# Kernel optimization log

Measured on AMD Instinct MI355X. Metric: run time of the kernel, lower is better.

## Reference

```python
import jax, jax.numpy as jnp
import numpy as np

B, RES, DIM, H, KD = 16, 32, 768, 12, 64
N = RES * RES          # 1024 tokens
D = KD                 # attn_ratio = 1 -> per-head value dim == key_dim
DH = D * H             # 768
SCALE = KD ** -0.5
LN_EPS = 1e-5


def _bias_idxs():
    # replicate the itertools.product construction: for row-major points,
    # offsets (|dy|,|dx|) are first seen in order dy-major, so id = |dy|*RES + |dx|
    coords = np.arange(N)
    y, x = coords // RES, coords % RES
    dy = np.abs(y[:, None] - y[None, :])
    dx = np.abs(x[:, None] - x[None, :])
    return jnp.asarray(dy * RES + dx, dtype=jnp.int32)  # [N, N]


def setup_inputs() -> dict:
    key = jax.random.key(0)
    ks = jax.random.split(key, 8)
    return {
        "x": jax.random.normal(ks[0], (B, N, DIM), jnp.float32),
        "ln_w": 1.0 + 0.01 * jax.random.normal(ks[1], (DIM,), jnp.float32),
        "ln_b": 0.01 * jax.random.normal(ks[2], (DIM,), jnp.float32),
        "qkv_w": 0.02 * jax.random.normal(ks[3], (3 * H * KD, DIM), jnp.float32),
        "qkv_b": 0.01 * jax.random.normal(ks[4], (3 * H * KD,), jnp.float32),
        "proj_w": 0.02 * jax.random.normal(ks[5], (DIM, DH), jnp.float32),
        "proj_b": 0.01 * jax.random.normal(ks[6], (DIM,), jnp.float32),
        "attn_biases": 0.1 * jax.random.normal(ks[7], (H, RES * RES), jnp.float32),
        "bias_idxs": _bias_idxs(),
    }


def reference(x, ln_w, ln_b, qkv_w, qkv_b, proj_w, proj_b, attn_biases, bias_idxs):
    # LayerNorm over the feature dim
    mu = jnp.mean(x, axis=-1, keepdims=True)
    var = jnp.mean(jnp.square(x - mu), axis=-1, keepdims=True)
    xn = (x - mu) * jax.lax.rsqrt(var + LN_EPS) * ln_w + ln_b

    # fused qkv projection -> [B, N, H, 3*KD], split per head
    qkv = (xn @ qkv_w.T + qkv_b).reshape(B, N, H, 3 * KD)
    q, k, v = jnp.split(qkv, [KD, 2 * KD], axis=3)  # each [B, N, H, KD]

    # gathered relative-position bias: [H, N, N]
    bias = attn_biases[:, bias_idxs]

    # scores + bias -> softmax -> AV
    attn = jnp.einsum("bnhk,bmhk->bhnm", q, k) * SCALE + bias[None]
    attn = jax.nn.softmax(attn, axis=-1)
    out = jnp.einsum("bhnm,bmhd->bnhd", attn, v).reshape(B, N, DH)
    return out @ proj_w.T + proj_b
```

## Files before the change

### kernel.cpp

```cpp
#include <hip/hip_runtime.h>
#include <cstdint>
#include <cstddef>

#define AS1 __attribute__((address_space(1)))
#define AS3 __attribute__((address_space(3)))

typedef float f32x4 __attribute__((ext_vector_type(4)));
typedef __bf16 bf16x8 __attribute__((ext_vector_type(8)));
typedef __bf16 bf16x4 __attribute__((ext_vector_type(4)));
typedef uint32_t u32x4 __attribute__((ext_vector_type(4)));

__device__ __forceinline__ void async_cp16(void* lds, const void* g) {
    __builtin_amdgcn_global_load_lds((AS1 void*)(g), (AS3 void*)(lds), 16, 0, 0);
}

__device__ __forceinline__ bf16x8 frag_of(u32x4 u) {
    return __builtin_bit_cast(bf16x8, u);
}

__global__ __launch_bounds__(256)
void cvt_w(const float* __restrict__ qkvw, const float* __restrict__ projw,
           __bf16* __restrict__ qkvwb, __bf16* __restrict__ projwb) {
    int i = blockIdx.x * 256 + threadIdx.x;
    if (i < 442368) {
        int row = i / 192, c4 = (i - row * 192) * 4;
        int t = (row >= 1536) ? 2 : (row >= 768 ? 1 : 0);
        int rem = row - t * 768;
        int hh = rem >> 6, d = rem & 63;
        int in_row = hh * 192 + t * 64 + d;
        float4 v = *(const float4*)(qkvw + (long)in_row * 768 + c4);
        bf16x4 o;
        o[0] = (__bf16)v.x; o[1] = (__bf16)v.y; o[2] = (__bf16)v.z; o[3] = (__bf16)v.w;
        *(bf16x4*)(qkvwb + (long)row * 768 + c4) = o;
    } else {
        int j = i - 442368;
        float4 v = ((const float4*)projw)[j];
        bf16x4 o;
        o[0] = (__bf16)v.x; o[1] = (__bf16)v.y; o[2] = (__bf16)v.z; o[3] = (__bf16)v.w;
        ((bf16x4*)projwb)[j] = o;
    }
}

__global__ __launch_bounds__(256)
void ln_kernel(const float* __restrict__ x, const float* __restrict__ w,
               const float* __restrict__ bsh, __bf16* __restrict__ xn) {
    const int lane = threadIdx.x & 63;
    const long row = (long)blockIdx.x * 4 + (threadIdx.x >> 6);
    const float4* xr = (const float4*)(x + row * 768);
    float4 v[3];
    v[0] = xr[lane]; v[1] = xr[lane + 64]; v[2] = xr[lane + 128];
    float s = 0.f, ss = 0.f;
#pragma unroll
    for (int i = 0; i < 3; ++i) {
        s  += v[i].x + v[i].y + v[i].z + v[i].w;
        ss += v[i].x * v[i].x + v[i].y * v[i].y + v[i].z * v[i].z + v[i].w * v[i].w;
    }
#pragma unroll
    for (int m = 1; m < 64; m <<= 1) { s += __shfl_xor(s, m); ss += __shfl_xor(ss, m); }
    const float mean = s * (1.f / 768.f);
    const float rstd = rsqrtf(ss * (1.f / 768.f) - mean * mean + 1e-5f);
    const float4* wv = (const float4*)w;
    const float4* bv = (const float4*)bsh;
    bf16x4* outp = (bf16x4*)(xn + row * 768);
#pragma unroll
    for (int i = 0; i < 3; ++i) {
        float4 wi = wv[lane + 64 * i], bi = bv[lane + 64 * i];
        bf16x4 o;
        o[0] = (__bf16)((v[i].x - mean) * rstd * wi.x + bi.x);
        o[1] = (__bf16)((v[i].y - mean) * rstd * wi.y + bi.y);
        o[2] = (__bf16)((v[i].z - mean) * rstd * wi.z + bi.z);
        o[3] = (__bf16)((v[i].w - mean) * rstd * wi.w + bi.w);
        outp[lane + 64 * i] = o;
    }
}

template <int MODE>
__device__ __forceinline__
void gemm_core(__bf16* As, __bf16* Bs,
               const __bf16* __restrict__ A, const __bf16* __restrict__ Bw,
               const float* __restrict__ bias,
               __bf16* __restrict__ q_out, __bf16* __restrict__ k_out,
               __bf16* __restrict__ vt_out, float* __restrict__ f_out,
               long bm, long bn) {
    constexpr int K = 768;
    const int tid  = threadIdx.x;
    const int lane = tid & 63;
    const int quad = lane >> 4;
    const int l16  = lane & 15;
    const int wave = tid >> 6;
    const int wm = wave >> 1, wn = wave & 1;

    const __bf16* Ab = A  + bm * K;
    const __bf16* Bb = Bw + bn * K;

    const int el0 = tid, el1 = tid + 256;
    const int rA0 = el0 >> 2, rA1 = el1 >> 2;
    const int kc  = (tid & 3) * 8;

    f32x4 acc[4][4] = {};

    for (int k0 = 0; k0 < K; k0 += 32) {
        __syncthreads();
        async_cp16((char*)As + el0 * 16, Ab + (long)rA0 * K + (k0 + kc));
        async_cp16((char*)As + el1 * 16, Ab + (long)rA1 * K + (k0 + kc));
        async_cp16((char*)Bs + el0 * 16, Bb + (long)rA0 * K + (k0 + kc));
        async_cp16((char*)Bs + el1 * 16, Bb + (long)rA1 * K + (k0 + kc));
        __syncthreads();

        const u32x4* Av = (const u32x4*)As;
        const u32x4* Bv = (const u32x4*)Bs;
        bf16x8 af[4], bfr[4];
#pragma unroll
        for (int t = 0; t < 4; ++t) {
            af[t]  = frag_of(Av[(wm * 64 + t * 16 + l16) * 4 + quad]);
            bfr[t] = frag_of(Bv[(wn * 64 + t * 16 + l16) * 4 + quad]);
        }
#pragma unroll
        for (int i = 0; i < 4; ++i)
#pragma unroll
            for (int j = 0; j < 4; ++j) {
                if constexpr (MODE == 0)
                    acc[i][j] = __builtin_amdgcn_mfma_f32_16x16x32_bf16(bfr[j], af[i], acc[i][j], 0, 0, 0);
                else
                    acc[i][j] = __builtin_amdgcn_mfma_f32_16x16x32_bf16(af[i], bfr[j], acc[i][j], 0, 0, 0);
            }
    }

    if constexpr (MODE == 0) {
#pragma unroll
        for (int j = 0; j < 4; ++j) {
            int col0 = (int)bn + wn * 64 + j * 16 + quad * 4;
            int t  = col0 >= 768;
            int cc = col0 - t * 768;
            int h  = cc >> 6, d = cc & 63;
            int f  = h * 192 + t * 64 + d;
            float4 bb = *(const float4*)(bias + f);
            __bf16* dst = t ? k_out : q_out;
#pragma unroll
            for (int i = 0; i < 4; ++i) {
                long row = bm + wm * 64 + i * 16 + l16;
                long b   = row >> 10;
                long n   = row & 1023;
                bf16x4 pk;
                pk[0] = (__bf16)(acc[i][j][0] + bb.x);
                pk[1] = (__bf16)(acc[i][j][1] + bb.y);
                pk[2] = (__bf16)(acc[i][j][2] + bb.z);
                pk[3] = (__bf16)(acc[i][j][3] + bb.w);
                *(bf16x4*)(dst + ((b * 12 + h) * 1024 + n) * 64 + d) = pk;
            }
        }
    } else if constexpr (MODE == 2) {
#pragma unroll
        for (int j = 0; j < 4; ++j) {
            int cv = (int)bn - 1536 + wn * 64 + j * 16 + l16;
            int h  = cv >> 6, d = cv & 63;
            float bv = bias[h * 192 + 128 + d];
#pragma unroll
            for (int i = 0; i < 4; ++i) {
                long row0 = bm + wm * 64 + i * 16 + quad * 4;
                long b    = row0 >> 10;
                long n0   = row0 & 1023;
                bf16x4 pk;
                pk[0] = (__bf16)(acc[i][j][0] + bv);
                pk[1] = (__bf16)(acc[i][j][1] + bv);
                pk[2] = (__bf16)(acc[i][j][2] + bv);
                pk[3] = (__bf16)(acc[i][j][3] + bv);
                *(bf16x4*)(vt_out + ((b * 12 + h) * 64 + d) * 1024 + n0) = pk;
            }
        }
    } else {
#pragma unroll
        for (int i = 0; i < 4; ++i) {
#pragma unroll
            for (int r = 0; r < 4; ++r) {
                long row = bm + wm * 64 + i * 16 + quad * 4 + r;
#pragma unroll
                for (int j = 0; j < 4; ++j) {
                    int col = (int)bn + wn * 64 + j * 16 + l16;
                    f_out[row * 768 + col] = acc[i][j][r] + bias[col];
                }
            }
        }
    }
}

__global__ __launch_bounds__(256, 2)
void gemm_qkv(const __bf16* __restrict__ A, const __bf16* __restrict__ Bw,
              const float* __restrict__ bias, __bf16* __restrict__ qb,
              __bf16* __restrict__ kb, __bf16* __restrict__ vtb) {
    __shared__ __align__(16) __bf16 As[128 * 32];
    __shared__ __align__(16) __bf16 Bs[128 * 32];
    int blk = blockIdx.x;
    int bx = blk % 18;
    long by = blk / 18;
    if (bx < 12)
        gemm_core<0>(As, Bs, A, Bw, bias, qb, kb, nullptr, nullptr, by * 128, (long)bx * 128);
    else
        gemm_core<2>(As, Bs, A, Bw, bias, nullptr, nullptr, vtb, nullptr, by * 128, (long)bx * 128);
}

__global__ __launch_bounds__(256, 2)
void gemm_proj(const __bf16* __restrict__ A, const __bf16* __restrict__ Bw,
               const float* __restrict__ bias, float* __restrict__ out) {
    __shared__ __align__(16) __bf16 As[128 * 32];
    __shared__ __align__(16) __bf16 Bs[128 * 32];
    gemm_core<1>(As, Bs, A, Bw, bias, nullptr, nullptr, nullptr, out,
                 (long)blockIdx.y * 128, (long)blockIdx.x * 128);
}

__global__ __launch_bounds__(256, 4)
void attn_kernel(const __bf16* __restrict__ Q, const __bf16* __restrict__ Kb,
                 const __bf16* __restrict__ Vt, const float* __restrict__ biases,
                 __bf16* __restrict__ out) {
    __shared__ __align__(16) __bf16 QPs[128 * 64];
    __shared__ __align__(16) __bf16 Ks[64 * 64];
    __shared__ __align__(16) __bf16 Vts[64 * 64];
    __shared__ __align__(16) float brow[1024];

    const int tid  = threadIdx.x;
    const int lane = tid & 63;
    const int wave = tid >> 6;
    const int quad = lane >> 4;
    const int l16  = lane & 15;
    const int sw   = l16 & 7;
    const int qt = blockIdx.x;
    const int h  = blockIdx.y;
    const int b  = blockIdx.z;

    const long bh = (long)b * 12 + h;
    const __bf16* Qg  = Q  + (bh * 1024 + qt * 128) * 64;
    const __bf16* Kg  = Kb + bh * 1024 * 64;
    const __bf16* Vtg = Vt + bh * 64 * 1024;

#pragma unroll
    for (int p = 0; p < 4; ++p) {
        int e = tid + p * 256, r = e >> 3, c = (e & 7) ^ (r & 7);
        async_cp16((char*)QPs + e * 16, Qg + r * 64 + c * 8);
    }
    {
        const float LOG2E = 1.4426950408889634f;
        float4 v = ((const float4*)(biases + (long)h * 1024))[tid];
        float4 o; o.x = v.x * LOG2E; o.y = v.y * LOG2E; o.z = v.z * LOG2E; o.w = v.w * LOG2E;
        ((float4*)brow)[tid] = o;
    }
    __syncthreads();

    bf16x8 aq[2][2];
    {
        const u32x4* Qv = (const u32x4*)QPs;
#pragma unroll
        for (int g = 0; g < 2; ++g) {
            int qrow = wave * 32 + g * 16 + l16;
            aq[g][0] = frag_of(Qv[qrow * 8 + (quad ^ sw)]);
            aq[g][1] = frag_of(Qv[qrow * 8 + ((quad + 4) ^ sw)]);
        }
    }

    const int yq = qt * 4 + wave;
    int pdxb[2][2][4];
#pragma unroll
    for (int g = 0; g < 2; ++g)
#pragma unroll
        for (int i2 = 0; i2 < 2; ++i2)
#pragma unroll
            for (int r = 0; r < 4; ++r) {
                int d = (g * 16 + l16) - (i2 * 16 + quad * 4 + r);
                pdxb[g][i2][r] = (d < 0 ? -d : d) * 4;
            }

    const float SSCALE = 0.125f * 1.4426950408889634f;
    float lacc[2] = {0.f, 0.f};
    f32x4 o[2][4] = {};
    __bf16* Psw = QPs + wave * 2048;

    const int e0 = tid, e1 = tid + 256;
    const int r0 = e0 >> 3, c0 = (e0 & 7) ^ (r0 & 7);
    const int r1 = e1 >> 3, c1 = (e1 & 7) ^ (r1 & 7);

    for (int kt = 0; kt < 16; ++kt) {
        __syncthreads();
        {
            const __bf16* Kt  = Kg + kt * 4096;
            const __bf16* Vtt = Vtg + kt * 64;
            async_cp16((char*)Ks + e0 * 16, Kt + r0 * 64 + c0 * 8);
            async_cp16((char*)Ks + e1 * 16, Kt + r1 * 64 + c1 * 8);
            async_cp16((char*)Vts + e0 * 16, Vtt + r0 * 1024 + c0 * 8);
            async_cp16((char*)Vts + e1 * 16, Vtt + r1 * 1024 + c1 * 8);
        }
        __syncthreads();

        f32x4 s[2][4];
        const u32x4* Kv = (const u32x4*)Ks;
#pragma unroll
        for (int nt = 0; nt < 4; ++nt) {
            int krow = nt * 16 + l16;
            bf16x8 k0 = frag_of(Kv[krow * 8 + (quad ^ sw)]);
            bf16x8 k1 = frag_of(Kv[krow * 8 + ((quad + 4) ^ sw)]);
#pragma unroll
            for (int g = 0; g < 2; ++g) {
                f32x4 z = {0.f, 0.f, 0.f, 0.f};
                z = __builtin_amdgcn_mfma_f32_16x16x32_bf16(k0, aq[g][0], z, 0, 0, 0);
                z = __builtin_amdgcn_mfma_f32_16x16x32_bf16(k1, aq[g][1], z, 0, 0, 0);
                s[g][nt] = z;
            }
        }

        int dy0 = yq - 2 * kt;     dy0 = dy0 < 0 ? -dy0 : dy0;
        int dy1 = yq - 2 * kt - 1; dy1 = dy1 < 0 ? -dy1 : dy1;
        const char* br0 = (const char*)(brow + dy0 * 32);
        const char* br1 = (const char*)(brow + dy1 * 32);
#pragma unroll
        for (int g = 0; g < 2; ++g) {
            int rowb = (g * 16 + l16) * 128 + (quad & 1) * 8;
#pragma unroll
            for (int nt = 0; nt < 4; ++nt) {
                const char* br = (nt & 2) ? br1 : br0;
                bf16x4 pk;
#pragma unroll
                for (int r = 0; r < 4; ++r) {
                    float bvv = *(const float*)(br + pdxb[g][nt & 1][r]);
                    float p = __builtin_amdgcn_exp2f(s[g][nt][r] * SSCALE + bvv);
                    lacc[g] += p;
                    pk[r] = (__bf16)p;
                }
                *(bf16x4*)((char*)Psw + rowb + (((nt * 2 + (quad >> 1)) ^ sw) << 4)) = pk;
            }
        }

        const u32x4* Pv = (const u32x4*)Psw;
        const u32x4* Vv = (const u32x4*)Vts;
        bf16x8 bp[2][2];
#pragma unroll
        for (int g = 0; g < 2; ++g) {
            int prow = g * 16 + l16;
            bp[g][0] = frag_of(Pv[prow * 8 + (quad ^ sw)]);
            bp[g][1] = frag_of(Pv[prow * 8 + ((quad + 4) ^ sw)]);
        }
#pragma unroll
        for (int dt = 0; dt < 4; ++dt) {
            int vrow = dt * 16 + l16;
            bf16x8 v0 = frag_of(Vv[vrow * 8 + (quad ^ sw)]);
            bf16x8 v1 = frag_of(Vv[vrow * 8 + ((quad + 4) ^ sw)]);
#pragma unroll
            for (int g = 0; g < 2; ++g) {
                o[g][dt] = __builtin_amdgcn_mfma_f32_16x16x32_bf16(v0, bp[g][0], o[g][dt], 0, 0, 0);
                o[g][dt] = __builtin_amdgcn_mfma_f32_16x16x32_bf16(v1, bp[g][1], o[g][dt], 0, 0, 0);
            }
        }
    }

#pragma unroll
    for (int g = 0; g < 2; ++g) {
        float l = lacc[g];
        l += __shfl_xor(l, 16);
        l += __shfl_xor(l, 32);
        const float rl = 1.f / l;
        const long n = qt * 128 + wave * 32 + g * 16 + l16;
        __bf16* op = out + ((long)b * 1024 + n) * 768 + h * 64 + quad * 4;
#pragma unroll
        for (int dt = 0; dt < 4; ++dt) {
            bf16x4 ov;
            ov[0] = (__bf16)(o[g][dt][0] * rl);
            ov[1] = (__bf16)(o[g][dt][1] * rl);
            ov[2] = (__bf16)(o[g][dt][2] * rl);
            ov[3] = (__bf16)(o[g][dt][3] * rl);
            *(bf16x4*)(op + dt * 16) = ov;
        }
    }
}

extern "C" void kernel_launch(void* const* d_in, const int* in_sizes, int n_in,
                              void* d_out, int out_size, void* d_ws, size_t ws_size,
                              hipStream_t stream) {
    (void)in_sizes; (void)n_in; (void)out_size; (void)ws_size;
    const float* x      = (const float*)d_in[0];
    const float* ln_w   = (const float*)d_in[1];
    const float* ln_b   = (const float*)d_in[2];
    const float* qkv_w  = (const float*)d_in[3];
    const float* qkv_b  = (const float*)d_in[4];
    const float* proj_w = (const float*)d_in[5];
    const float* proj_b = (const float*)d_in[6];
    const float* ab     = (const float*)d_in[7];
    float* outp = (float*)d_out;

    char* ws = (char*)d_ws;
    __bf16* xn     = (__bf16*)(ws);
    __bf16* aout   = (__bf16*)(ws);
    __bf16* qkvwb  = (__bf16*)(ws + 25165824);
    __bf16* projwb = (__bf16*)(ws + 28704768);
    __bf16* qb     = (__bf16*)(ws + 29884416);
    __bf16* kb     = (__bf16*)(ws + 55050240);
    __bf16* vtb    = (__bf16*)(ws + 80216064);

    cvt_w<<<2304, 256, 0, stream>>>(qkv_w, proj_w, qkvwb, projwb);
    ln_kernel<<<4096, 256, 0, stream>>>(x, ln_w, ln_b, xn);
    gemm_qkv<<<2304, 256, 0, stream>>>(xn, qkvwb, qkv_b, qb, kb, vtb);
    attn_kernel<<<dim3(8, 12, 16), 256, 0, stream>>>(qb, kb, vtb, ab, aout);
    gemm_proj<<<dim3(6, 128), 256, 0, stream>>>(aout, projwb, proj_b, outp);
}
```

Measured before the change: 348.3 us.

## Halve attention query tile to 64 rows, store bias in fp16, raise occupancy bounds

The attention kernel now handles 64 query rows per block instead of 128, with each wave owning 16 rows, and the grid doubles to compensate. The per-head bias row moves from fp32 to fp16 in LDS, and the Q/P buffer is halved, cutting LDS and register use so launch bounds can rise to 6 blocks per CU. The GEMM launch bounds also go from 2 to 3 blocks. In exchange, each K/V tile loaded into LDS is reused by half as many queries, which doubles K/V traffic, and the fp16 bias adds a small rounding error.

After: 333.7 us. -4.2%, faster.

```diff
diff --git a/kernel.cpp b/kernel.cpp
--- a/kernel.cpp
+++ b/kernel.cpp
@@ -8,6 +8,7 @@
 typedef float f32x4 __attribute__((ext_vector_type(4)));
 typedef __bf16 bf16x8 __attribute__((ext_vector_type(8)));
 typedef __bf16 bf16x4 __attribute__((ext_vector_type(4)));
+typedef _Float16 h16x4 __attribute__((ext_vector_type(4)));
 typedef uint32_t u32x4 __attribute__((ext_vector_type(4)));
 
 __device__ __forceinline__ void async_cp16(void* lds, const void* g) {
@@ -184,7 +185,7 @@
     }
 }
 
-__global__ __launch_bounds__(256, 2)
+__global__ __launch_bounds__(256, 3)
 void gemm_qkv(const __bf16* __restrict__ A, const __bf16* __restrict__ Bw,
               const float* __restrict__ bias, __bf16* __restrict__ qb,
               __bf16* __restrict__ kb, __bf16* __restrict__ vtb) {
@@ -199,7 +200,7 @@
         gemm_core<2>(As, Bs, A, Bw, bias, nullptr, nullptr, vtb, nullptr, by * 128, (long)bx * 128);
 }
 
-__global__ __launch_bounds__(256, 2)
+__global__ __launch_bounds__(256, 3)
 void gemm_proj(const __bf16* __restrict__ A, const __bf16* __restrict__ Bw,
                const float* __restrict__ bias, float* __restrict__ out) {
     __shared__ __align__(16) __bf16 As[128 * 32];
@@ -208,14 +209,14 @@
                  (long)blockIdx.y * 128, (long)blockIdx.x * 128);
 }
 
-__global__ __launch_bounds__(256, 4)
+__global__ __launch_bounds__(256, 6)
 void attn_kernel(const __bf16* __restrict__ Q, const __bf16* __restrict__ Kb,
                  const __bf16* __restrict__ Vt, const float* __restrict__ biases,
                  __bf16* __restrict__ out) {
-    __shared__ __align__(16) __bf16 QPs[128 * 64];
+    __shared__ __align__(16) __bf16 QPs[64 * 64];
     __shared__ __align__(16) __bf16 Ks[64 * 64];
     __shared__ __align__(16) __bf16 Vts[64 * 64];
-    __shared__ __align__(16) float brow[1024];
+    __shared__ __align__(16) _Float16 brow[1024];
 
     const int tid  = threadIdx.x;
     const int lane = tid & 63;
@@ -228,54 +229,50 @@
     const int b  = blockIdx.z;
 
     const long bh = (long)b * 12 + h;
-    const __bf16* Qg  = Q  + (bh * 1024 + qt * 128) * 64;
+    const __bf16* Qg  = Q  + (bh * 1024 + qt * 64) * 64;
     const __bf16* Kg  = Kb + bh * 1024 * 64;
     const __bf16* Vtg = Vt + bh * 64 * 1024;
 
-#pragma unroll
-    for (int p = 0; p < 4; ++p) {
-        int e = tid + p * 256, r = e >> 3, c = (e & 7) ^ (r & 7);
-        async_cp16((char*)QPs + e * 16, Qg + r * 64 + c * 8);
-    }
+    const int e0 = tid, e1 = tid + 256;
+    const int r0 = e0 >> 3, c0 = (e0 & 7) ^ (r0 & 7);
+    const int r1 = e1 >> 3, c1 = (e1 & 7) ^ (r1 & 7);
+
+    async_cp16((char*)QPs + e0 * 16, Qg + r0 * 64 + c0 * 8);
+    async_cp16((char*)QPs + e1 * 16, Qg + r1 * 64 + c1 * 8);
     {
         const float LOG2E = 1.4426950408889634f;
         float4 v = ((const float4*)(biases + (long)h * 1024))[tid];
-        float4 o; o.x = v.x * LOG2E; o.y = v.y * LOG2E; o.z = v.z * LOG2E; o.w = v.w * LOG2E;
-        ((float4*)brow)[tid] = o;
+        h16x4 o;
+        o[0] = (_Float16)(v.x * LOG2E); o[1] = (_Float16)(v.y * LOG2E);
+        o[2] = (_Float16)(v.z * LOG2E); o[3] = (_Float16)(v.w * LOG2E);
+        *(h16x4*)(brow + tid * 4) = o;
     }
     __syncthreads();
 
-    bf16x8 aq[2][2];
+    bf16x8 aq[2];
     {
         const u32x4* Qv = (const u32x4*)QPs;
-#pragma unroll
-        for (int g = 0; g < 2; ++g) {
-            int qrow = wave * 32 + g * 16 + l16;
-            aq[g][0] = frag_of(Qv[qrow * 8 + (quad ^ sw)]);
-            aq[g][1] = frag_of(Qv[qrow * 8 + ((quad + 4) ^ sw)]);
-        }
-    }
-
-    const int yq = qt * 4 + wave;
-    int pdxb[2][2][4];
-#pragma unroll
-    for (int g = 0; g < 2; ++g)
-#pragma unroll
-        for (int i2 = 0; i2 < 2; ++i2)
-#pragma unroll
-            for (int r = 0; r < 4; ++r) {
-                int d = (g * 16 + l16) - (i2 * 16 + quad * 4 + r);
-                pdxb[g][i2][r] = (d < 0 ? -d : d) * 4;
-            }
+        int qrow = wave * 16 + l16;
+        aq[0] = frag_of(Qv[qrow * 8 + (quad ^ sw)]);
+        aq[1] = frag_of(Qv[qrow * 8 + ((quad + 4) ^ sw)]);
+    }
+
+    const int yq = 2 * qt + (wave >> 1);
+    const int xq = ((wave & 1) << 4) + l16;
+    int pdx[2][4];
+#pragma unroll
+    for (int i2 = 0; i2 < 2; ++i2)
+#pragma unroll
+        for (int r = 0; r < 4; ++r) {
+            int xk = (i2 << 4) + quad * 4 + r;
+            int d = xq - xk; pdx[i2][r] = d < 0 ? -d : d;
+        }
 
     const float SSCALE = 0.125f * 1.4426950408889634f;
-    float lacc[2] = {0.f, 0.f};
-    f32x4 o[2][4] = {};
-    __bf16* Psw = QPs + wave * 2048;
-
-    const int e0 = tid, e1 = tid + 256;
-    const int r0 = e0 >> 3, c0 = (e0 & 7) ^ (r0 & 7);
-    const int r1 = e1 >> 3, c1 = (e1 & 7) ^ (r1 & 7);
+    float lacc = 0.f;
+    f32x4 o[4] = {};
+    __bf16* Psw = QPs + wave * 1024;
+    const int pwb = l16 * 128 + (quad & 1) * 8;
 
     for (int kt = 0; kt < 16; ++kt) {
         __syncthreads();
@@ -289,83 +286,64 @@
         }
         __syncthreads();
 
-        f32x4 s[2][4];
+        f32x4 s[4];
         const u32x4* Kv = (const u32x4*)Ks;
 #pragma unroll
         for (int nt = 0; nt < 4; ++nt) {
             int krow = nt * 16 + l16;
             bf16x8 k0 = frag_of(Kv[krow * 8 + (quad ^ sw)]);
             bf16x8 k1 = frag_of(Kv[krow * 8 + ((quad + 4) ^ sw)]);
-#pragma unroll
-            for (int g = 0; g < 2; ++g) {
-                f32x4 z = {0.f, 0.f, 0.f, 0.f};
-                z = __builtin_amdgcn_mfma_f32_16x16x32_bf16(k0, aq[g][0], z, 0, 0, 0);
-                z = __builtin_amdgcn_mfma_f32_16x16x32_bf16(k1, aq[g][1], z, 0, 0, 0);
-                s[g][nt] = z;
-            }
+            f32x4 z = {0.f, 0.f, 0.f, 0.f};
+            z = __builtin_amdgcn_mfma_f32_16x16x32_bf16(k0, aq[0], z, 0, 0, 0);
+            z = __builtin_amdgcn_mfma_f32_16x16x32_bf16(k1, aq[1], z, 0, 0, 0);
+            s[nt] = z;
         }
 
         int dy0 = yq - 2 * kt;     dy0 = dy0 < 0 ? -dy0 : dy0;
         int dy1 = yq - 2 * kt - 1; dy1 = dy1 < 0 ? -dy1 : dy1;
-        const char* br0 = (const char*)(brow + dy0 * 32);
-        const char* br1 = (const char*)(brow + dy1 * 32);
-#pragma unroll
-        for (int g = 0; g < 2; ++g) {
-            int rowb = (g * 16 + l16) * 128 + (quad & 1) * 8;
-#pragma unroll
-            for (int nt = 0; nt < 4; ++nt) {
-                const char* br = (nt & 2) ? br1 : br0;
-                bf16x4 pk;
-#pragma unroll
-                for (int r = 0; r < 4; ++r) {
-                    float bvv = *(const float*)(br + pdxb[g][nt & 1][r]);
-                    float p = __builtin_amdgcn_exp2f(s[g][nt][r] * SSCALE + bvv);
-                    lacc[g] += p;
-                    pk[r] = (__bf16)p;
-                }
-                *(bf16x4*)((char*)Psw + rowb + (((nt * 2 + (quad >> 1)) ^ sw) << 4)) = pk;
-            }
+        const _Float16* br0 = brow + dy0 * 32;
+        const _Float16* br1 = brow + dy1 * 32;
+#pragma unroll
+        for (int nt = 0; nt < 4; ++nt) {
+            const _Float16* br = (nt & 2) ? br1 : br0;
+            bf16x4 pk;
+#pragma unroll
+            for (int r = 0; r < 4; ++r) {
+                float p = __builtin_amdgcn_exp2f(s[nt][r] * SSCALE + (float)br[pdx[nt & 1][r]]);
+                lacc += p;
+                pk[r] = (__bf16)p;
+            }
+            *(bf16x4*)((char*)Psw + pwb + (((nt * 2 + (quad >> 1)) ^ sw) << 4)) = pk;
         }
 
         const u32x4* Pv = (const u32x4*)Psw;
         const u32x4* Vv = (const u32x4*)Vts;
-        bf16x8 bp[2][2];
-#pragma unroll
-        for (int g = 0; g < 2; ++g) {
-            int prow = g * 16 + l16;
-            bp[g][0] = frag_of(Pv[prow * 8 + (quad ^ sw)]);
-            bp[g][1] = frag_of(Pv[prow * 8 + ((quad + 4) ^ sw)]);
-        }
+        bf16x8 bp0 = frag_of(Pv[l16 * 8 + (quad ^ sw)]);
+        bf16x8 bp1 = frag_of(Pv[l16 * 8 + ((quad + 4) ^ sw)]);
 #pragma unroll
         for (int dt = 0; dt < 4; ++dt) {
             int vrow = dt * 16 + l16;
             bf16x8 v0 = frag_of(Vv[vrow * 8 + (quad ^ sw)]);
             bf16x8 v1 = frag_of(Vv[vrow * 8 + ((quad + 4) ^ sw)]);
-#pragma unroll
-            for (int g = 0; g < 2; ++g) {
-                o[g][dt] = __builtin_amdgcn_mfma_f32_16x16x32_bf16(v0, bp[g][0], o[g][dt], 0, 0, 0);
-                o[g][dt] = __builtin_amdgcn_mfma_f32_16x16x32_bf16(v1, bp[g][1], o[g][dt], 0, 0, 0);
-            }
-        }
-    }
-
-#pragma unroll
-    for (int g = 0; g < 2; ++g) {
-        float l = lacc[g];
-        l += __shfl_xor(l, 16);
-        l += __shfl_xor(l, 32);
-        const float rl = 1.f / l;
-        const long n = qt * 128 + wave * 32 + g * 16 + l16;
-        __bf16* op = out + ((long)b * 1024 + n) * 768 + h * 64 + quad * 4;
-#pragma unroll
-        for (int dt = 0; dt < 4; ++dt) {
-            bf16x4 ov;
-            ov[0] = (__bf16)(o[g][dt][0] * rl);
-            ov[1] = (__bf16)(o[g][dt][1] * rl);
-            ov[2] = (__bf16)(o[g][dt][2] * rl);
-            ov[3] = (__bf16)(o[g][dt][3] * rl);
-            *(bf16x4*)(op + dt * 16) = ov;
-        }
+            o[dt] = __builtin_amdgcn_mfma_f32_16x16x32_bf16(v0, bp0, o[dt], 0, 0, 0);
+            o[dt] = __builtin_amdgcn_mfma_f32_16x16x32_bf16(v1, bp1, o[dt], 0, 0, 0);
+        }
+    }
+
+    lacc += __shfl_xor(lacc, 16);
+    lacc += __shfl_xor(lacc, 32);
+    const float rl = 1.f / lacc;
+
+    const long n = qt * 64 + wave * 16 + l16;
+    __bf16* op = out + ((long)b * 1024 + n) * 768 + h * 64 + quad * 4;
+#pragma unroll
+    for (int dt = 0; dt < 4; ++dt) {
+        bf16x4 ov;
+        ov[0] = (__bf16)(o[dt][0] * rl);
+        ov[1] = (__bf16)(o[dt][1] * rl);
+        ov[2] = (__bf16)(o[dt][2] * rl);
+        ov[3] = (__bf16)(o[dt][3] * rl);
+        *(bf16x4*)(op + dt * 16) = ov;
     }
 }
 
@@ -395,6 +373,6 @@
     cvt_w<<<2304, 256, 0, stream>>>(qkv_w, proj_w, qkvwb, projwb);
     ln_kernel<<<4096, 256, 0, stream>>>(x, ln_w, ln_b, xn);
     gemm_qkv<<<2304, 256, 0, stream>>>(xn, qkvwb, qkv_b, qb, kb, vtb);
-    attn_kernel<<<dim3(8, 12, 16), 256, 0, stream>>>(qb, kb, vtb, ab, aout);
+    attn_kernel<<<dim3(16, 12, 16), 256, 0, stream>>>(qb, kb, vtb, ab, aout);
     gemm_proj<<<dim3(6, 128), 256, 0, stream>>>(aout, projwb, proj_b, outp);
 }
```
